# Performance work log

Measured on AMD Instinct MI355X. Metric: run time of the kernel, lower is better.

The kernel has to match this reference:

```python
import jax, jax.numpy as jnp
import numpy as np
from jax.scipy.special import logsumexp

ROI_RADIUS = 0.1
TAU = 0.5
EPSILON = 1.0
K = 2
THRESH = 1e-4


def setup_inputs() -> dict:
    key = jax.random.key(0)
    k1, k2, k3, k4 = jax.random.split(key, 4)
    return {
        "adata1_embedding": jax.random.normal(k1, (4096, 256), jnp.float32),
        "adata2_embedding": jax.random.normal(k2, (4096, 256), jnp.float32),
        "adata1_loc": jax.random.uniform(k3, (4096, 2), jnp.float32),
        "adata2_loc": jax.random.uniform(k4, (4096, 2), jnp.float32),
        "iters": 100,
    }


def _normalize(x):
    n = jnp.linalg.norm(x, axis=-1, keepdims=True)
    return x / jnp.maximum(n, 1e-12)


def _get_scores(e1, e2, l1, l2):
    # torch.cdist(p=2) on [N,2] locations
    loc_dis = jnp.sqrt(jnp.sum((l1[:, None, :] - l2[None, :, :]) ** 2, axis=-1))
    roi_mask = jnp.where(loc_dis < ROI_RADIUS, 1.0, 0.0).astype(e1.dtype)
    cross = _normalize(e1) @ _normalize(e2).T  # cosine similarity [N1,N2]
    scores = roi_mask * ((cross + 1.0) / (2.0 * TAU + 1e-6))
    return scores[None]  # [1, N1, N2]


def _nonzero_median(scores):
    # torch.median over nonzero entries (lower median)
    flat = scores.reshape(-1)
    nz = flat != 0
    nnz = nz.sum()
    s = jnp.sort(jnp.where(nz, flat, jnp.inf))  # zeros pushed to the end
    return s[(nnz - 1) // 2]


def _log_sinkhorn(Z, log_mu, log_nu, iters):
    # u, v computed under no_grad in torch -> stop_gradient here
    Zc = jax.lax.stop_gradient(Z) / (EPSILON + 1e-6)
    lm = jax.lax.stop_gradient(log_mu)
    ln = jax.lax.stop_gradient(log_nu)

    def cond(state):
        _, _, i, err = state
        return jnp.logical_and(i < iters, err >= THRESH)

    def body(state):
        u, v, i, _ = state
        u1 = u
        u = lm - logsumexp(Zc + v[:, None, :], axis=2)
        v = ln - logsumexp(Zc + u[:, :, None], axis=1)
        err = jnp.abs(u - u1).sum(-1).mean()
        return (u, v, i + 1, err)

    u0 = jnp.zeros_like(lm)
    v0 = jnp.zeros_like(ln)
    u, v, _, _ = jax.lax.while_loop(cond, body, (u0, v0, 0, jnp.inf))
    return Z + u[:, :, None] + v[:, None, :]


def _log_optimal_transport(scores, bin_score, iters):
    b, m, n = scores.shape
    bins0 = jnp.full((b, m, 1), bin_score, scores.dtype)
    bins1 = jnp.full((b, 1, n), bin_score, scores.dtype)
    alpha = jnp.full((b, 1, 1), bin_score, scores.dtype)
    couplings = jnp.concatenate(
        [jnp.concatenate([scores, bins0], -1),
         jnp.concatenate([bins1, alpha], -1)], 1)  # [b, m+1, n+1]
    ms = jnp.float32(m)
    ns = jnp.float32(n)
    norm = -jnp.log(ms + ns)
    log_mu = jnp.concatenate([jnp.full((m,), norm), (jnp.log(ns) + norm)[None]])
    log_nu = jnp.concatenate([jnp.full((n,), norm), (jnp.log(ms) + norm)[None]])
    log_mu = jnp.broadcast_to(log_mu[None], (b, m + 1))
    log_nu = jnp.broadcast_to(log_nu[None], (b, n + 1))
    Z = _log_sinkhorn(couplings, log_mu, log_nu, iters)
    return Z - norm


def reference(adata1_embedding, adata2_embedding, adata1_loc, adata2_loc, iters):
    scores = _get_scores(adata1_embedding, adata2_embedding, adata1_loc, adata2_loc)
    bin_score = _nonzero_median(scores)
    soft = _log_optimal_transport(scores, bin_score, iters)  # [1, m+1, n+1]

    S = soft[:, :-1, :-1]
    b, m, n = S.shape
    vals0, idx0_all = jax.lax.top_k(S, K)                      # [1, m, K]
    vals1, idx1_all = jax.lax.top_k(jnp.swapaxes(S, 1, 2), K)  # [1, n, K]

    all_mscore0 = jnp.zeros((1, m), S.dtype)
    all_mscore1 = jnp.zeros((1, n), S.dtype)
    match0, match1 = [], []
    for k in range(K):
        i0 = idx0_all[..., k]  # [1, m], indices into n
        i1 = idx1_all[..., k]  # [1, n], indices into m
        mutual0 = jnp.arange(m)[None] == jnp.take_along_axis(i1, i0, axis=1)
        mutual1 = jnp.arange(n)[None] == jnp.take_along_axis(i0, i1, axis=1)
        ms0 = jnp.where(mutual0, jnp.exp(vals0[..., k]), 0.0)
        ms1 = jnp.where(mutual1, jnp.exp(vals1[..., k]), 0.0)
        all_mscore0 = all_mscore0 + ms0
        all_mscore1 = all_mscore1 + ms1
        valid0 = mutual0 & (ms0 > 0)
        valid1 = mutual1 & jnp.take_along_axis(valid0, i1, axis=1)
        match0.append(jnp.where(valid0, i0, -1)[0])
        match1.append(jnp.where(valid1, i1, -1)[0])

    indices0 = jnp.stack(match0)  # [K, m], -1 = unmatched
    indices1 = jnp.stack(match1)  # [K, n]
    return soft, all_mscore0, all_mscore1, indices0, indices1
```

## Files before the change

kernel.cpp:

```cpp
#include <hip/hip_runtime.h>
#include <cstdint>
#include <cstddef>
#include <math.h>

constexpr int N = 4096;
constexpr int D = 256;
constexpr int N1 = N + 1;
constexpr int MAXNZ = 256;
constexpr int SBLK = 64;
constexpr double SNAP_THETA = 3e-6;
constexpr double CONV_EPS = 1e-9;

constexpr size_t OFF_SOFT = 0;
constexpr size_t OFF_MS0  = (size_t)N1 * N1;
constexpr size_t OFF_MS1  = OFF_MS0 + N;
constexpr size_t OFF_IDX0 = OFF_MS1 + N;
constexpr size_t OFF_IDX1 = OFF_IDX0 + 2 * (size_t)N;

struct Ws {
  double vals_r[(size_t)N * MAXNZ];
  double vals_c[(size_t)N * MAXNZ];
  int    cols_r[(size_t)N * MAXNZ];
  int    rows_c[(size_t)N * MAXNZ];
  double inv1[N], inv2[N];
  int    cnt_r[N], cnt_c[N];
  double u[N1], v[N1], expu[N1], expv[N1];
  double partA[SBLK], partB[SBLK], partE[SBLK];
  int    flags[SBLK * 16];
  int    nnzTotal;
  unsigned long long medPrefix;
  int    medK;
  double binScore, bcz;
  int    hist[8 * 256];
  double vals0[N * 2], vals1[N * 2];
  int    idx0[N * 2], idx1[N * 2];
  int    valid0[2 * N];
  double evals_r[(size_t)N * MAXNZ];
  double evals_c[(size_t)N * MAXNZ];
};

__device__ __forceinline__ double wsum64d(double x) {
  #pragma unroll
  for (int m = 1; m < 64; m <<= 1) x += __shfl_xor(x, m, 64);
  return x;
}
__device__ __forceinline__ void ag_store(double* p, double x) {
  __hip_atomic_store(p, x, __ATOMIC_RELAXED, __HIP_MEMORY_SCOPE_AGENT);
}
__device__ __forceinline__ double ag_load(const double* p) {
  return __hip_atomic_load(p, __ATOMIC_RELAXED, __HIP_MEMORY_SCOPE_AGENT);
}

__global__ void k_init(Ws* ws) {
  int tid = threadIdx.x;
  for (int i = tid; i < N1; i += 256) {
    ws->u[i] = 0.0; ws->v[i] = 0.0; ws->expu[i] = 1.0; ws->expv[i] = 1.0;
  }
  for (int i = tid; i < N; i += 256) ws->cnt_c[i] = 0;
  for (int i = tid; i < 8 * 256; i += 256) ws->hist[i] = 0;
  for (int i = tid; i < SBLK * 16; i += 256) ws->flags[i] = 0;
  if (tid == 0) {
    ws->nnzTotal = 0; ws->medPrefix = 0ull; ws->medK = 0;
  }
}

__global__ void k_norms(const float* e1, const float* e2, Ws* ws) {
  int tid = threadIdx.x, lane = tid & 63, wid = tid >> 6;
  int r = blockIdx.x * 4 + wid;
  if (r >= 2 * N) return;
  const float* p = (r < N) ? (e1 + (size_t)r * D) : (e2 + (size_t)(r - N) * D);
  double s = 0.0;
  #pragma unroll
  for (int k = lane; k < D; k += 64) { double x = (double)p[k]; s += x * x; }
  s = wsum64d(s);
  if (lane == 0) {
    double invn = 1.0 / fmax(sqrt(s), 1e-12);
    if (r < N) ws->inv1[r] = invn; else ws->inv2[r - N] = invn;
  }
}

__global__ void k_build(const float* e1, const float* e2,
                        const float* l1, const float* l2, Ws* ws, int wr_evals) {
  __shared__ float erow[D];
  __shared__ int hcols[256];
  __shared__ int wcnt[4];
  __shared__ int s_hcnt;
  int self = blockIdx.x;
  int tid = threadIdx.x, lane = tid & 63, wid = tid >> 6;
  erow[tid] = e1[(size_t)self * D + tid];
  float sx = l1[self * 2];
  float sy = l1[self * 2 + 1];
  double invs = ws->inv1[self];
  size_t base = (size_t)self * MAXNZ;
  int written = 0;
  __syncthreads();
  for (int c0 = 0; c0 < N; c0 += 256) {
    int j = c0 + tid;
    float dx = sx - l2[j * 2];
    float dy = sy - l2[j * 2 + 1];
    float dist = sqrtf(dx * dx + dy * dy);
    bool in = dist < 0.1f;
    unsigned long long m = __ballot(in);
    int rank = __popcll(m & ((1ull << lane) - 1ull));
    if (lane == 0) wcnt[wid] = (int)__popcll(m);
    __syncthreads();
    int wb = 0;
    for (int w = 0; w < wid; ++w) wb += wcnt[w];
    if (in) hcols[wb + rank] = j;
    if (tid == 0) s_hcnt = wcnt[0] + wcnt[1] + wcnt[2] + wcnt[3];
    __syncthreads();
    int hc = s_hcnt;
    for (int h = wid; h < hc; h += 4) {
      int j2 = hcols[h];
      const float* po = e2 + (size_t)j2 * D;
      double acc = 0.0;
      #pragma unroll
      for (int k = lane; k < D; k += 64) acc += (double)erow[k] * (double)po[k];
      acc = wsum64d(acc);
      if (lane == 0) {
        double cross = (acc * invs) * ws->inv2[j2];
        double val = (cross + 1.0) / 1.000001;
        int slot = written + h;
        if (slot < MAXNZ) {
          ws->vals_r[base + slot] = val;
          ws->cols_r[base + slot] = j2;
          if (wr_evals) ws->evals_r[base + slot] = expm1(val / 1.000001);
        }
      }
    }
    written += hc;
    __syncthreads();
  }
  if (tid == 0) {
    int cnt = min(written, MAXNZ);
    ws->cnt_r[self] = cnt;
    atomicAdd(&ws->nnzTotal, cnt);
  }
}

__global__ void k_transpose(Ws* ws, int wr_evals) {
  int r = blockIdx.x;
  int cnt = ws->cnt_r[r];
  size_t base = (size_t)r * MAXNZ;
  for (int e = threadIdx.x; e < cnt; e += 256) {
    int c = ws->cols_r[base + e];
    int slot = atomicAdd(&ws->cnt_c[c], 1);
    if (slot < MAXNZ) {
      size_t cb = (size_t)c * MAXNZ + slot;
      ws->vals_c[cb] = ws->vals_r[base + e];
      ws->rows_c[cb] = r;
      if (wr_evals) ws->evals_c[cb] = ws->evals_r[base + e];
    }
  }
}
__global__ void k_clampc(Ws* ws) {
  int c = blockIdx.x * blockDim.x + threadIdx.x;
  if (c < N && ws->cnt_c[c] > MAXNZ) ws->cnt_c[c] = MAXNZ;
}

__global__ void k_hist(Ws* ws, int round) {
  __shared__ int lh[256];
  lh[threadIdx.x] = 0;
  __syncthreads();
  int shift = 56 - 8 * round;
  unsigned long long prefix = ws->medPrefix;
  unsigned long long hm = (round == 0) ? 0ull : (~0ull << (shift + 8));
  int total = N * MAXNZ;
  for (int s = blockIdx.x * blockDim.x + threadIdx.x; s < total; s += gridDim.x * blockDim.x) {
    int row = s >> 8, e = s & (MAXNZ - 1);
    if (e < ws->cnt_r[row]) {
      unsigned long long bits = __double_as_longlong(ws->vals_r[(size_t)row * MAXNZ + e]);
      if ((bits & hm) == (prefix & hm)) atomicAdd(&lh[(int)((bits >> shift) & 255)], 1);
    }
  }
  __syncthreads();
  if (lh[threadIdx.x]) atomicAdd(&ws->hist[round * 256 + threadIdx.x], lh[threadIdx.x]);
}

__global__ void k_select(Ws* ws, int round) {
  __shared__ int cum[256];
  int tid = threadIdx.x;
  if (round == 0 && tid == 0) ws->medK = (ws->nnzTotal - 1) >> 1;
  __syncthreads();
  int k = ws->medK;
  int h = ws->hist[round * 256 + tid];
  cum[tid] = h;
  __syncthreads();
  for (int off = 1; off < 256; off <<= 1) {
    int val = (tid >= off) ? cum[tid - off] : 0;
    __syncthreads();
    cum[tid] += val;
    __syncthreads();
  }
  int below = cum[tid] - h;
  if (cum[tid] > k && below <= k) {
    int shift = 56 - 8 * round;
    unsigned long long p = ws->medPrefix | ((unsigned long long)tid << shift);
    ws->medPrefix = p;
    ws->medK = k - below;
    if (round == 7) {
      double bs = __longlong_as_double(p);
      ws->binScore = bs;
      ws->bcz = bs / 1.000001;
    }
  }
}

__device__ __forceinline__ void gbar(Ws* ws, int gen) {
  __syncthreads();
  if (threadIdx.x < 64) {
    if (threadIdx.x == 0)
      __hip_atomic_store(&ws->flags[blockIdx.x * 16], gen, __ATOMIC_RELEASE, __HIP_MEMORY_SCOPE_AGENT);
    int f;
    do {
      f = __hip_atomic_load(&ws->flags[threadIdx.x * 16], __ATOMIC_ACQUIRE, __HIP_MEMORY_SCOPE_AGENT);
    } while (f < gen);
  }
  __syncthreads();
}

__global__ __launch_bounds__(1024) void k_sink(Ws* ws, const int* d_iters, int use_evals) {
  const int tid = threadIdx.x, lane = tid & 63, wid = tid >> 6;
  const int gw = blockIdx.x * 16 + wid;
  const int NW = 1024;
  const int iters = d_iters[0];
  const double norm0 = -log(8192.0);
  const double bcz = ws->bcz;
  __shared__ double s_ev[N];
  __shared__ double s_part[16], s_partE[16];
  __shared__ double s_scalar, s_scalarE;
  double Sv = 4096.0;
  double v4096 = 0.0;

  for (int t = 0; t < iters; ++t) {
    if (t == 0) {
      for (int c = tid; c < N; c += 1024) s_ev[c] = ag_load(&ws->expv[c]);
      v4096 = ag_load(&ws->v[N]);
      __syncthreads();
    }
    double ebv = exp(bcz + v4096);

    double eu_acc = 0.0, de_acc = 0.0;
    for (int row = gw; row <= N; row += NW) {
      if (row < N) {
        int cnt = ws->cnt_r[row];
        size_t base = (size_t)row * MAXNZ;
        double acc = 0.0;
        if (use_evals) {
          for (int e = lane; e < cnt; e += 64)
            acc += ws->evals_r[base + e] * s_ev[ws->cols_r[base + e]];
        } else {
          for (int e = lane; e < cnt; e += 64)
            acc += expm1(ws->vals_r[base + e] / 1.000001) * s_ev[ws->cols_r[base + e]];
        }
        acc = wsum64d(acc);
        double unew = norm0 - log(Sv + acc + ebv);
        if (lane == 0) {
          double uold = ag_load(&ws->u[row]);
          de_acc += fabs(unew - uold);
          ag_store(&ws->u[row], unew);
          double eu = exp(unew);
          ag_store(&ws->expu[row], eu);
          eu_acc += eu;
        }
      } else {
        double unew = (log(4096.0) + norm0) - bcz - log(Sv + exp(v4096));
        if (lane == 0) {
          double uold = ag_load(&ws->u[N]);
          de_acc += fabs(unew - uold);
          ag_store(&ws->u[row], unew);
        }
      }
    }
    if (lane == 0) { s_part[wid] = eu_acc; s_partE[wid] = de_acc; }
    __syncthreads();
    if (tid == 0) {
      double p = 0.0, pe = 0.0;
      #pragma unroll
      for (int w = 0; w < 16; ++w) { p += s_part[w]; pe += s_partE[w]; }
      ag_store(&ws->partA[blockIdx.x], p);
      ag_store(&ws->partE[blockIdx.x], pe);
    }
    gbar(ws, 2 * t + 1);
    for (int r = tid; r < N; r += 1024) s_ev[r] = ag_load(&ws->expu[r]);
    double u4096 = ag_load(&ws->u[N]);
    if (wid == 0) {
      double p = ag_load(&ws->partA[lane]);
      double pe = ag_load(&ws->partE[lane]);
      p = wsum64d(p);
      pe = wsum64d(pe);
      if (lane == 0) { s_scalar = p; s_scalarE = pe; }
    }
    __syncthreads();
    double Su = s_scalar;
    double errU = s_scalarE;
    double ebu = exp(bcz + u4096);

    double ev_acc = 0.0;
    for (int col = gw; col <= N; col += NW) {
      if (col < N) {
        int cnt = ws->cnt_c[col];
        size_t base = (size_t)col * MAXNZ;
        double acc = 0.0;
        if (use_evals) {
          for (int e = lane; e < cnt; e += 64)
            acc += ws->evals_c[base + e] * s_ev[ws->rows_c[base + e]];
        } else {
          for (int e = lane; e < cnt; e += 64)
            acc += expm1(ws->vals_c[base + e] / 1.000001) * s_ev[ws->rows_c[base + e]];
        }
        acc = wsum64d(acc);
        double vnew = norm0 - log(Su + acc + ebu);
        if (lane == 0) {
          ag_store(&ws->v[col], vnew);
          double ev = exp(vnew);
          ag_store(&ws->expv[col], ev);
          ev_acc += ev;
        }
      } else {
        double vnew = (log(4096.0) + norm0) - bcz - log(Su + exp(u4096));
        if (lane == 0) ag_store(&ws->v[col], vnew);
      }
    }
    if (lane == 0) s_part[wid] = ev_acc;
    __syncthreads();
    if (tid == 0) {
      double p = 0.0;
      #pragma unroll
      for (int w = 0; w < 16; ++w) p += s_part[w];
      ag_store(&ws->partB[blockIdx.x], p);
    }
    gbar(ws, 2 * t + 2);
    for (int c = tid; c < N; c += 1024) s_ev[c] = ag_load(&ws->expv[c]);
    v4096 = ag_load(&ws->v[N]);
    if (wid == 0) {
      double p = ag_load(&ws->partB[lane]);
      p = wsum64d(p);
      if (lane == 0) s_scalar = p;
    }
    __syncthreads();
    Sv = s_scalar;

    if (errU < CONV_EPS) break;
  }
}

__global__ void k_soft(Ws* ws, float* out) {
  __shared__ double srow[N];
  int i = blockIdx.x, tid = threadIdx.x;
  double norm0 = -log(8192.0);
  double bs = ws->binScore;
  if (i < N) {
    for (int j = tid; j < N; j += 256) srow[j] = 0.0;
    __syncthreads();
    int cnt = ws->cnt_r[i];
    size_t base = (size_t)i * MAXNZ;
    for (int e = tid; e < cnt; e += 256) srow[ws->cols_r[base + e]] = ws->vals_r[base + e];
    __syncthreads();
    double ui = ws->u[i];
    size_t ob = (size_t)i * N1;
    for (int j = tid; j < N; j += 256) out[ob + j] = (float)(((srow[j] + ui) + ws->v[j]) - norm0);
    if (tid == 0) out[ob + N] = (float)(((bs + ui) + ws->v[N]) - norm0);
  } else {
    double un = ws->u[N];
    size_t ob = (size_t)N * N1;
    for (int j = tid; j < N; j += 256) out[ob + j] = (float)(((bs + un) + ws->v[j]) - norm0);
    if (tid == 0) out[ob + N] = (float)(((bs + un) + ws->v[N]) - norm0);
  }
}

struct T3 { double v1, v2, v3; int i1, i2, i3; };
__device__ __forceinline__ bool betterD(double a, int ia, double b, int ib) {
  return a > b || (a == b && ia < ib);
}
__device__ __forceinline__ void insT3(T3& t, double nv, int ni) {
  if (betterD(nv, ni, t.v1, t.i1)) { t.v3 = t.v2; t.i3 = t.i2; t.v2 = t.v1; t.i2 = t.i1; t.v1 = nv; t.i1 = ni; }
  else if (betterD(nv, ni, t.v2, t.i2)) { t.v3 = t.v2; t.i3 = t.i2; t.v2 = nv; t.i2 = ni; }
  else if (betterD(nv, ni, t.v3, t.i3)) { t.v3 = nv; t.i3 = ni; }
}

template <bool COL>
__global__ void k_top2(Ws* ws) {
  __shared__ double sval[N];
  __shared__ T3 red[256];
  int i = blockIdx.x, tid = threadIdx.x;
  double norm0 = -log(8192.0);
  for (int j = tid; j < N; j += 256) sval[j] = 0.0;
  __syncthreads();
  int cnt = COL ? ws->cnt_c[i] : ws->cnt_r[i];
  size_t base = (size_t)i * MAXNZ;
  const int* idxs = COL ? ws->rows_c : ws->cols_r;
  const double* vls = COL ? ws->vals_c : ws->vals_r;
  for (int e = tid; e < cnt; e += 256) sval[idxs[base + e]] = vls[base + e];
  __syncthreads();
  double fixedUV = COL ? ws->v[i] : ws->u[i];
  T3 t; t.v1 = -INFINITY; t.v2 = -INFINITY; t.v3 = -INFINITY;
  t.i1 = 0x7fffffff; t.i2 = 0x7fffffff; t.i3 = 0x7fffffff;
  for (int j = tid; j < N; j += 256) {
    double val = COL ? (((sval[j] + ws->u[j]) + fixedUV) - norm0)
                     : (((sval[j] + fixedUV) + ws->v[j]) - norm0);
    insT3(t, val, j);
  }
  red[tid] = t;
  __syncthreads();
  for (int off = 128; off > 0; off >>= 1) {
    if (tid < off) {
      T3 a = red[tid];
      T3 b = red[tid + off];
      insT3(a, b.v1, b.i1);
      insT3(a, b.v2, b.i2);
      insT3(a, b.v3, b.i3);
      red[tid] = a;
    }
    __syncthreads();
  }
  if (tid == 0) {
    T3 a = red[0];
    if (a.v2 - a.v3 < SNAP_THETA && a.i3 < a.i2) { double tv = a.v2; int ti = a.i2; a.v2 = a.v3; a.i2 = a.i3; a.v3 = tv; a.i3 = ti; }
    if (a.v1 - a.v2 < SNAP_THETA && a.i2 < a.i1) { double tv = a.v1; int ti = a.i1; a.v1 = a.v2; a.i1 = a.i2; a.v2 = tv; a.i2 = ti; }
    if (a.v2 - a.v3 < SNAP_THETA && a.i3 < a.i2) { double tv = a.v2; int ti = a.i2; a.v2 = a.v3; a.i2 = a.i3; a.v3 = tv; a.i3 = ti; }
    if (COL) {
      ws->vals1[i * 2] = a.v1; ws->idx1[i * 2] = a.i1;
      ws->vals1[i * 2 + 1] = a.v2; ws->idx1[i * 2 + 1] = a.i2;
    } else {
      ws->vals0[i * 2] = a.v1; ws->idx0[i * 2] = a.i1;
      ws->vals0[i * 2 + 1] = a.v2; ws->idx0[i * 2 + 1] = a.i2;
    }
  }
}

__global__ void k_match0(Ws* ws, float* out) {
  int r = blockIdx.x * blockDim.x + threadIdx.x;
  if (r >= N) return;
  double msum = 0.0;
  #pragma unroll
  for (int k = 0; k < 2; ++k) {
    int c = ws->idx0[r * 2 + k];
    bool mutual = (ws->idx1[c * 2 + k] == r);
    double ms = mutual ? exp(ws->vals0[r * 2 + k]) : 0.0;
    msum += ms;
    bool valid = mutual && (ms > 0.0);
    ws->valid0[k * N + r] = valid ? 1 : 0;
    out[OFF_IDX0 + (size_t)k * N + r] = valid ? (float)c : -1.0f;
  }
  out[OFF_MS0 + r] = (float)msum;
}

__global__ void k_match1(Ws* ws, float* out) {
  int c = blockIdx.x * blockDim.x + threadIdx.x;
  if (c >= N) return;
  double msum = 0.0;
  #pragma unroll
  for (int k = 0; k < 2; ++k) {
    int r = ws->idx1[c * 2 + k];
    bool mutual = (ws->idx0[r * 2 + k] == c);
    double ms = mutual ? exp(ws->vals1[c * 2 + k]) : 0.0;
    msum += ms;
    bool valid = mutual && (ws->valid0[k * N + r] != 0);
    out[OFF_IDX1 + (size_t)k * N + c] = valid ? (float)r : -1.0f;
  }
  out[OFF_MS1 + c] = (float)msum;
}

extern "C" void kernel_launch(void* const* d_in, const int* in_sizes, int n_in,
                              void* d_out, int out_size, void* d_ws, size_t ws_size,
                              hipStream_t stream) {
  const float* e1 = (const float*)d_in[0];
  const float* e2 = (const float*)d_in[1];
  const float* l1 = (const float*)d_in[2];
  const float* l2 = (const float*)d_in[3];
  const int* iters = (const int*)d_in[4];
  float* out = (float*)d_out;
  Ws* ws = (Ws*)d_ws;
  int use_evals = (ws_size >= sizeof(Ws)) ? 1 : 0;

  k_init<<<1, 256, 0, stream>>>(ws);
  k_norms<<<2048, 256, 0, stream>>>(e1, e2, ws);
  k_build<<<N, 256, 0, stream>>>(e1, e2, l1, l2, ws, use_evals);
  k_transpose<<<N, 256, 0, stream>>>(ws, use_evals);
  k_clampc<<<16, 256, 0, stream>>>(ws);
  for (int r = 0; r < 8; ++r) {
    k_hist<<<1024, 256, 0, stream>>>(ws, r);
    k_select<<<1, 256, 0, stream>>>(ws, r);
  }
  k_sink<<<SBLK, 1024, 0, stream>>>(ws, iters, use_evals);
  k_soft<<<N1, 256, 0, stream>>>(ws, out);
  k_top2<false><<<N, 256, 0, stream>>>(ws);
  k_top2<true><<<N, 256, 0, stream>>>(ws);
  k_match0<<<16, 256, 0, stream>>>(ws, out);
  k_match1<<<16, 256, 0, stream>>>(ws, out);
}
```

Baseline: 957.2 us.

## Fuse median radix rounds into one persistent kernel, merge row top2 into soft

Replaces the 16 histogram/select launches of the radix-select median with a single 64-block persistent kernel that uses a software grid barrier between rounds. The row top-2 search moves into k_soft so the row-wise score is computed once, and the clamp kernel becomes inline min() at the points where counts are read. k_build now runs 512 threads per block over 512-column chunks. The aim is to cut launch count and redundant passes. The cost is that the median histogram now runs on only 64 blocks, and correctness relies on co-residency for the spin barrier.

```diff
diff --git a/kernel.cpp b/kernel.cpp
--- a/kernel.cpp
+++ b/kernel.cpp
@@ -27,6 +27,7 @@
   double u[N1], v[N1], expu[N1], expv[N1];
   double partA[SBLK], partB[SBLK], partE[SBLK];
   int    flags[SBLK * 16];
+  int    flags2[SBLK * 16];
   int    nnzTotal;
   unsigned long long medPrefix;
   int    medK;
@@ -58,7 +59,7 @@
   }
   for (int i = tid; i < N; i += 256) ws->cnt_c[i] = 0;
   for (int i = tid; i < 8 * 256; i += 256) ws->hist[i] = 0;
-  for (int i = tid; i < SBLK * 16; i += 256) ws->flags[i] = 0;
+  for (int i = tid; i < SBLK * 16; i += 256) { ws->flags[i] = 0; ws->flags2[i] = 0; }
   if (tid == 0) {
     ws->nnzTotal = 0; ws->medPrefix = 0ull; ws->medK = 0;
   }
@@ -82,19 +83,19 @@
 __global__ void k_build(const float* e1, const float* e2,
                         const float* l1, const float* l2, Ws* ws, int wr_evals) {
   __shared__ float erow[D];
-  __shared__ int hcols[256];
-  __shared__ int wcnt[4];
+  __shared__ int hcols[512];
+  __shared__ int wcnt[8];
   __shared__ int s_hcnt;
   int self = blockIdx.x;
   int tid = threadIdx.x, lane = tid & 63, wid = tid >> 6;
-  erow[tid] = e1[(size_t)self * D + tid];
+  if (tid < D) erow[tid] = e1[(size_t)self * D + tid];
   float sx = l1[self * 2];
   float sy = l1[self * 2 + 1];
   double invs = ws->inv1[self];
   size_t base = (size_t)self * MAXNZ;
   int written = 0;
   __syncthreads();
-  for (int c0 = 0; c0 < N; c0 += 256) {
+  for (int c0 = 0; c0 < N; c0 += 512) {
     int j = c0 + tid;
     float dx = sx - l2[j * 2];
     float dy = sy - l2[j * 2 + 1];
@@ -107,10 +108,15 @@
     int wb = 0;
     for (int w = 0; w < wid; ++w) wb += wcnt[w];
     if (in) hcols[wb + rank] = j;
-    if (tid == 0) s_hcnt = wcnt[0] + wcnt[1] + wcnt[2] + wcnt[3];
+    if (tid == 0) {
+      int sH = 0;
+      #pragma unroll
+      for (int w = 0; w < 8; ++w) sH += wcnt[w];
+      s_hcnt = sH;
+    }
     __syncthreads();
     int hc = s_hcnt;
-    for (int h = wid; h < hc; h += 4) {
+    for (int h = wid; h < hc; h += 8) {
       int j2 = hcols[h];
       const float* po = e2 + (size_t)j2 * D;
       double acc = 0.0;
@@ -153,56 +159,69 @@
     }
   }
 }
-__global__ void k_clampc(Ws* ws) {
-  int c = blockIdx.x * blockDim.x + threadIdx.x;
-  if (c < N && ws->cnt_c[c] > MAXNZ) ws->cnt_c[c] = MAXNZ;
-}
-
-__global__ void k_hist(Ws* ws, int round) {
+
+__device__ __forceinline__ void gbar2(Ws* ws, int gen) {
+  __syncthreads();
+  if (threadIdx.x < 64) {
+    if (threadIdx.x == 0)
+      __hip_atomic_store(&ws->flags2[blockIdx.x * 16], gen, __ATOMIC_RELEASE, __HIP_MEMORY_SCOPE_AGENT);
+    int f;
+    do {
+      f = __hip_atomic_load(&ws->flags2[threadIdx.x * 16], __ATOMIC_ACQUIRE, __HIP_MEMORY_SCOPE_AGENT);
+    } while (f < gen);
+  }
+  __syncthreads();
+}
+
+__global__ void k_median(Ws* ws) {
   __shared__ int lh[256];
-  lh[threadIdx.x] = 0;
-  __syncthreads();
-  int shift = 56 - 8 * round;
-  unsigned long long prefix = ws->medPrefix;
-  unsigned long long hm = (round == 0) ? 0ull : (~0ull << (shift + 8));
-  int total = N * MAXNZ;
-  for (int s = blockIdx.x * blockDim.x + threadIdx.x; s < total; s += gridDim.x * blockDim.x) {
-    int row = s >> 8, e = s & (MAXNZ - 1);
-    if (e < ws->cnt_r[row]) {
-      unsigned long long bits = __double_as_longlong(ws->vals_r[(size_t)row * MAXNZ + e]);
-      if ((bits & hm) == (prefix & hm)) atomicAdd(&lh[(int)((bits >> shift) & 255)], 1);
-    }
-  }
-  __syncthreads();
-  if (lh[threadIdx.x]) atomicAdd(&ws->hist[round * 256 + threadIdx.x], lh[threadIdx.x]);
-}
-
-__global__ void k_select(Ws* ws, int round) {
   __shared__ int cum[256];
   int tid = threadIdx.x;
-  if (round == 0 && tid == 0) ws->medK = (ws->nnzTotal - 1) >> 1;
-  __syncthreads();
-  int k = ws->medK;
-  int h = ws->hist[round * 256 + tid];
-  cum[tid] = h;
-  __syncthreads();
-  for (int off = 1; off < 256; off <<= 1) {
-    int val = (tid >= off) ? cum[tid - off] : 0;
-    __syncthreads();
-    cum[tid] += val;
-    __syncthreads();
-  }
-  int below = cum[tid] - h;
-  if (cum[tid] > k && below <= k) {
+  int gen = 0;
+  for (int round = 0; round < 8; ++round) {
+    lh[tid] = 0;
+    __syncthreads();
     int shift = 56 - 8 * round;
-    unsigned long long p = ws->medPrefix | ((unsigned long long)tid << shift);
-    ws->medPrefix = p;
-    ws->medK = k - below;
-    if (round == 7) {
-      double bs = __longlong_as_double(p);
-      ws->binScore = bs;
-      ws->bcz = bs / 1.000001;
-    }
+    unsigned long long prefix =
+        __hip_atomic_load(&ws->medPrefix, __ATOMIC_RELAXED, __HIP_MEMORY_SCOPE_AGENT);
+    unsigned long long hm = (round == 0) ? 0ull : (~0ull << (shift + 8));
+    int total = N * MAXNZ;
+    for (int s = blockIdx.x * 256 + tid; s < total; s += SBLK * 256) {
+      int row = s >> 8, e = s & (MAXNZ - 1);
+      if (e < ws->cnt_r[row]) {
+        unsigned long long bits = __double_as_longlong(ws->vals_r[(size_t)row * MAXNZ + e]);
+        if ((bits & hm) == (prefix & hm)) atomicAdd(&lh[(int)((bits >> shift) & 255)], 1);
+      }
+    }
+    __syncthreads();
+    if (lh[tid]) atomicAdd(&ws->hist[round * 256 + tid], lh[tid]);
+    gbar2(ws, ++gen);
+    if (blockIdx.x == 0) {
+      if (round == 0 && tid == 0) ws->medK = (ws->nnzTotal - 1) >> 1;
+      __syncthreads();
+      int k = ws->medK;
+      int h = __hip_atomic_load(&ws->hist[round * 256 + tid], __ATOMIC_RELAXED, __HIP_MEMORY_SCOPE_AGENT);
+      cum[tid] = h;
+      __syncthreads();
+      for (int off = 1; off < 256; off <<= 1) {
+        int val = (tid >= off) ? cum[tid - off] : 0;
+        __syncthreads();
+        cum[tid] += val;
+        __syncthreads();
+      }
+      int below = cum[tid] - h;
+      if (cum[tid] > k && below <= k) {
+        unsigned long long p = prefix | ((unsigned long long)tid << shift);
+        __hip_atomic_store(&ws->medPrefix, p, __ATOMIC_RELAXED, __HIP_MEMORY_SCOPE_AGENT);
+        ws->medK = k - below;
+        if (round == 7) {
+          double bs = __longlong_as_double((long long)p);
+          ws->binScore = bs;
+          ws->bcz = bs / 1.000001;
+        }
+      }
+    }
+    gbar2(ws, ++gen);
   }
 }
 
@@ -299,7 +318,7 @@
     double ev_acc = 0.0;
     for (int col = gw; col <= N; col += NW) {
       if (col < N) {
-        int cnt = ws->cnt_c[col];
+        int cnt = min(ws->cnt_c[col], MAXNZ);
         size_t base = (size_t)col * MAXNZ;
         double acc = 0.0;
         if (use_evals) {
@@ -345,8 +364,24 @@
   }
 }
 
+struct T3 { double v1, v2, v3; int i1, i2, i3; };
+__device__ __forceinline__ bool betterD(double a, int ia, double b, int ib) {
+  return a > b || (a == b && ia < ib);
+}
+__device__ __forceinline__ void insT3(T3& t, double nv, int ni) {
+  if (betterD(nv, ni, t.v1, t.i1)) { t.v3 = t.v2; t.i3 = t.i2; t.v2 = t.v1; t.i2 = t.i1; t.v1 = nv; t.i1 = ni; }
+  else if (betterD(nv, ni, t.v2, t.i2)) { t.v3 = t.v2; t.i3 = t.i2; t.v2 = nv; t.i2 = ni; }
+  else if (betterD(nv, ni, t.v3, t.i3)) { t.v3 = nv; t.i3 = ni; }
+}
+__device__ __forceinline__ void snapT3(T3& a) {
+  if (a.v2 - a.v3 < SNAP_THETA && a.i3 < a.i2) { double tv = a.v2; int ti = a.i2; a.v2 = a.v3; a.i2 = a.i3; a.v3 = tv; a.i3 = ti; }
+  if (a.v1 - a.v2 < SNAP_THETA && a.i2 < a.i1) { double tv = a.v1; int ti = a.i1; a.v1 = a.v2; a.i1 = a.i2; a.v2 = tv; a.i2 = ti; }
+  if (a.v2 - a.v3 < SNAP_THETA && a.i3 < a.i2) { double tv = a.v2; int ti = a.i2; a.v2 = a.v3; a.i2 = a.i3; a.v3 = tv; a.i3 = ti; }
+}
+
 __global__ void k_soft(Ws* ws, float* out) {
   __shared__ double srow[N];
+  __shared__ T3 red[256];
   int i = blockIdx.x, tid = threadIdx.x;
   double norm0 = -log(8192.0);
   double bs = ws->binScore;
@@ -359,8 +394,33 @@
     __syncthreads();
     double ui = ws->u[i];
     size_t ob = (size_t)i * N1;
-    for (int j = tid; j < N; j += 256) out[ob + j] = (float)(((srow[j] + ui) + ws->v[j]) - norm0);
+    T3 t; t.v1 = -INFINITY; t.v2 = -INFINITY; t.v3 = -INFINITY;
+    t.i1 = 0x7fffffff; t.i2 = 0x7fffffff; t.i3 = 0x7fffffff;
+    for (int j = tid; j < N; j += 256) {
+      double val = ((srow[j] + ui) + ws->v[j]) - norm0;
+      out[ob + j] = (float)val;
+      insT3(t, val, j);
+    }
     if (tid == 0) out[ob + N] = (float)(((bs + ui) + ws->v[N]) - norm0);
+    red[tid] = t;
+    __syncthreads();
+    for (int off = 128; off > 0; off >>= 1) {
+      if (tid < off) {
+        T3 a = red[tid];
+        T3 b = red[tid + off];
+        insT3(a, b.v1, b.i1);
+        insT3(a, b.v2, b.i2);
+        insT3(a, b.v3, b.i3);
+        red[tid] = a;
+      }
+      __syncthreads();
+    }
+    if (tid == 0) {
+      T3 a = red[0];
+      snapT3(a);
+      ws->vals0[i * 2] = a.v1; ws->idx0[i * 2] = a.i1;
+      ws->vals0[i * 2 + 1] = a.v2; ws->idx0[i * 2 + 1] = a.i2;
+    }
   } else {
     double un = ws->u[N];
     size_t ob = (size_t)N * N1;
@@ -369,36 +429,22 @@
   }
 }
 
-struct T3 { double v1, v2, v3; int i1, i2, i3; };
-__device__ __forceinline__ bool betterD(double a, int ia, double b, int ib) {
-  return a > b || (a == b && ia < ib);
-}
-__device__ __forceinline__ void insT3(T3& t, double nv, int ni) {
-  if (betterD(nv, ni, t.v1, t.i1)) { t.v3 = t.v2; t.i3 = t.i2; t.v2 = t.v1; t.i2 = t.i1; t.v1 = nv; t.i1 = ni; }
-  else if (betterD(nv, ni, t.v2, t.i2)) { t.v3 = t.v2; t.i3 = t.i2; t.v2 = nv; t.i2 = ni; }
-  else if (betterD(nv, ni, t.v3, t.i3)) { t.v3 = nv; t.i3 = ni; }
-}
-
-template <bool COL>
-__global__ void k_top2(Ws* ws) {
+__global__ void k_top2c(Ws* ws) {
   __shared__ double sval[N];
   __shared__ T3 red[256];
   int i = blockIdx.x, tid = threadIdx.x;
   double norm0 = -log(8192.0);
   for (int j = tid; j < N; j += 256) sval[j] = 0.0;
   __syncthreads();
-  int cnt = COL ? ws->cnt_c[i] : ws->cnt_r[i];
+  int cnt = min(ws->cnt_c[i], MAXNZ);
   size_t base = (size_t)i * MAXNZ;
-  const int* idxs = COL ? ws->rows_c : ws->cols_r;
-  const double* vls = COL ? ws->vals_c : ws->vals_r;
-  for (int e = tid; e < cnt; e += 256) sval[idxs[base + e]] = vls[base + e];
-  __syncthreads();
-  double fixedUV = COL ? ws->v[i] : ws->u[i];
+  for (int e = tid; e < cnt; e += 256) sval[ws->rows_c[base + e]] = ws->vals_c[base + e];
+  __syncthreads();
+  double fixedUV = ws->v[i];
   T3 t; t.v1 = -INFINITY; t.v2 = -INFINITY; t.v3 = -INFINITY;
   t.i1 = 0x7fffffff; t.i2 = 0x7fffffff; t.i3 = 0x7fffffff;
   for (int j = tid; j < N; j += 256) {
-    double val = COL ? (((sval[j] + ws->u[j]) + fixedUV) - norm0)
-                     : (((sval[j] + fixedUV) + ws->v[j]) - norm0);
+    double val = (((sval[j] + ws->u[j]) + fixedUV) - norm0);
     insT3(t, val, j);
   }
   red[tid] = t;
@@ -416,16 +462,9 @@
   }
   if (tid == 0) {
     T3 a = red[0];
-    if (a.v2 - a.v3 < SNAP_THETA && a.i3 < a.i2) { double tv = a.v2; int ti = a.i2; a.v2 = a.v3; a.i2 = a.i3; a.v3 = tv; a.i3 = ti; }
-    if (a.v1 - a.v2 < SNAP_THETA && a.i2 < a.i1) { double tv = a.v1; int ti = a.i1; a.v1 = a.v2; a.i1 = a.i2; a.v2 = tv; a.i2 = ti; }
-    if (a.v2 - a.v3 < SNAP_THETA && a.i3 < a.i2) { double tv = a.v2; int ti = a.i2; a.v2 = a.v3; a.i2 = a.i3; a.v3 = tv; a.i3 = ti; }
-    if (COL) {
-      ws->vals1[i * 2] = a.v1; ws->idx1[i * 2] = a.i1;
-      ws->vals1[i * 2 + 1] = a.v2; ws->idx1[i * 2 + 1] = a.i2;
-    } else {
-      ws->vals0[i * 2] = a.v1; ws->idx0[i * 2] = a.i1;
-      ws->vals0[i * 2 + 1] = a.v2; ws->idx0[i * 2 + 1] = a.i2;
-    }
+    snapT3(a);
+    ws->vals1[i * 2] = a.v1; ws->idx1[i * 2] = a.i1;
+    ws->vals1[i * 2 + 1] = a.v2; ws->idx1[i * 2 + 1] = a.i2;
   }
 }
 
@@ -476,17 +515,12 @@
 
   k_init<<<1, 256, 0, stream>>>(ws);
   k_norms<<<2048, 256, 0, stream>>>(e1, e2, ws);
-  k_build<<<N, 256, 0, stream>>>(e1, e2, l1, l2, ws, use_evals);
+  k_build<<<N, 512, 0, stream>>>(e1, e2, l1, l2, ws, use_evals);
   k_transpose<<<N, 256, 0, stream>>>(ws, use_evals);
-  k_clampc<<<16, 256, 0, stream>>>(ws);
-  for (int r = 0; r < 8; ++r) {
-    k_hist<<<1024, 256, 0, stream>>>(ws, r);
-    k_select<<<1, 256, 0, stream>>>(ws, r);
-  }
+  k_median<<<SBLK, 256, 0, stream>>>(ws);
   k_sink<<<SBLK, 1024, 0, stream>>>(ws, iters, use_evals);
   k_soft<<<N1, 256, 0, stream>>>(ws, out);
-  k_top2<false><<<N, 256, 0, stream>>>(ws);
-  k_top2<true><<<N, 256, 0, stream>>>(ws);
+  k_top2c<<<N, 256, 0, stream>>>(ws);
   k_match0<<<16, 256, 0, stream>>>(ws, out);
   k_match1<<<16, 256, 0, stream>>>(ws, out);
 }
```

Measured after the change: 1.046 ms. 1.09x slower.
